# Kernel optimization log

Measured on AMD Instinct MI355X. Metric: run time of the kernel, lower is better.

The kernel has to match this reference:

```python
import jax, jax.numpy as jnp
import numpy as np

N, D, C = 12288, 64, 3
K, GAMMA = 85, 0.5
SAMPLE = 2000


def _safe_sqrt(sq):
    # sqrt with zero gradient at exactly-zero inputs (matches torch cdist/norm backward)
    sq = jnp.maximum(sq, 0.0)
    return jnp.where(sq > 0, jnp.sqrt(jnp.where(sq > 0, sq, 1.0)), 0.0)


def _cdist(a, b):
    # pairwise euclidean distances [Na, Nb]
    sq = jnp.sum(a * a, -1)[:, None] + jnp.sum(b * b, -1)[None, :] - 2.0 * (a @ b.T)
    return _safe_sqrt(sq)


def setup_inputs() -> dict:
    key = jax.random.key(0)
    k1, k2 = jax.random.split(key)
    return {
        "embeddings": jax.random.normal(k1, (N, D), dtype=jnp.float32),
        "coords": jax.random.normal(k2, (N, C), dtype=jnp.float32),
    }


def reference(embeddings, coords):
    n = embeddings.shape[0]
    sample_size = min(n, SAMPLE)
    # deterministic stand-in for torch.randperm sampling
    idx = jax.random.permutation(jax.random.key(42), n)[:sample_size]
    emb_s = embeddings[idx]
    coord_s = coords[idx]

    # Pearson correlation between flattened sample distance matrices
    ed = _cdist(emb_s, emb_s).ravel()
    cd = _cdist(coord_s, coord_s).ravel()
    ec = ed - ed.mean()
    cc = cd - cd.mean()
    es = jnp.sqrt((ec * ec).mean() + 1e-8)
    cs = jnp.sqrt((cc * cc).mean() + 1e-8)
    pearson = (ec * cc).mean() / (es * cs + 1e-8)
    pearson_loss = 1.0 - pearson

    k = min(K, n - 1)
    # KNN in coordinate space, no grad (torch.no_grad)
    coords_ng = jax.lax.stop_gradient(coords)
    full = _cdist(coords_ng, coords_ng)               # [N, N]
    _, knn_idx = jax.lax.top_k(-full, k + 1)          # smallest distances
    knn_idx = knn_idx[:, 1:]                          # drop self -> [N, k]

    nb_emb = embeddings[knn_idx]                      # [N, k, D]
    nb_coord = coords[knn_idx]                        # [N, k, C]
    pred_dist = _safe_sqrt(jnp.sum((embeddings[:, None, :] - nb_emb) ** 2, -1))  # [N, k]
    true_dist = _safe_sqrt(jnp.sum((coords[:, None, :] - nb_coord) ** 2, -1))    # [N, k]
    decay_weight = jnp.exp(-GAMMA * true_dist)
    local_loss = jnp.mean((pred_dist - true_dist) ** 2 * decay_weight)

    return pearson_loss + 0.5 * local_loss
```

## Files before the change

### kernel.cpp

```cpp
#include <hip/hip_runtime.h>
#include <math.h>

#define NPTS 12288
#define DIM 64
#define KNN 85
#define KSEL 86
#define SAMPLE 2000
#define SSTRIDE 6
#define GAMMA 0.5f
#define NT 256
#define WPB 4
#define VIT 12
#define NV 48
#define VCAP 256
#define PT 64
#define PPITCH 68
#define PBLK 1024


struct PearsonS {
  float EqT[DIM][PPITCH];
  float Cp[PT][4];
  float Cq[PT][4];
  float np_[PT];
  float nq_[PT];
  double wred[WPB][5];
};
struct KnnS {
  unsigned h[256];
  unsigned bmax[WPB];
  unsigned long long vkey[VCAP];
  unsigned long long thrkey;
  unsigned vcnt;
};
union SharedU { PearsonS p; KnnS k; };

__global__ void prep_kernel(const float* __restrict__ coord,
                            float* __restrict__ cx, float* __restrict__ cy,
                            float* __restrict__ cz) {
  int j = blockIdx.x * 256 + threadIdx.x;
  if (j < NPTS) {
    cx[j] = coord[3 * j];
    cy[j] = coord[3 * j + 1];
    cz[j] = coord[3 * j + 2];
  }
}

__device__ __forceinline__ void pearson_body(
    SharedU& sh, const float* __restrict__ emb, const float* __restrict__ coord,
    double* __restrict__ acc) {
  const int tid = threadIdx.x;
  const int tx = tid & 15, ty = tid >> 4;
  const int lane = tid & 63, wv = tid >> 6;
  const int pb = blockIdx.x;
  const int p0 = (pb >> 5) * PT, q0 = (pb & 31) * PT;

  for (int e = tid; e < PT * DIM; e += 256) {
    int r = e >> 6, k = e & 63;
    int gq = (q0 + r < SAMPLE ? q0 + r : 0) * SSTRIDE;
    sh.p.EqT[k][r] = emb[(size_t)gq * DIM + k];
  }
  if (tid < PT) {
    int g = (p0 + tid < SAMPLE ? p0 + tid : 0) * SSTRIDE;
    sh.p.Cp[tid][0] = coord[3 * g]; sh.p.Cp[tid][1] = coord[3 * g + 1]; sh.p.Cp[tid][2] = coord[3 * g + 2];
    const float4* E4 = (const float4*)(emb + (size_t)g * DIM);
    float a = 0.f;
    #pragma unroll
    for (int k4 = 0; k4 < DIM / 4; ++k4) {
      float4 v = E4[k4];
      a += v.x * v.x; a += v.y * v.y; a += v.z * v.z; a += v.w * v.w;
    }
    sh.p.np_[tid] = a;
  } else if (tid < 2 * PT) {
    int r = tid - PT;
    int g = (q0 + r < SAMPLE ? q0 + r : 0) * SSTRIDE;
    sh.p.Cq[r][0] = coord[3 * g]; sh.p.Cq[r][1] = coord[3 * g + 1]; sh.p.Cq[r][2] = coord[3 * g + 2];
    const float4* E4 = (const float4*)(emb + (size_t)g * DIM);
    float a = 0.f;
    #pragma unroll
    for (int k4 = 0; k4 < DIM / 4; ++k4) {
      float4 v = E4[k4];
      a += v.x * v.x; a += v.y * v.y; a += v.z * v.z; a += v.w * v.w;
    }
    sh.p.nq_[r] = a;
  }
  __syncthreads();

  const float* rp0; const float* rp1; const float* rp2; const float* rp3;
  {
    int r0 = p0 + 4 * ty;
    int g0 = (r0     < SAMPLE ? r0     : 0) * SSTRIDE;
    int g1 = (r0 + 1 < SAMPLE ? r0 + 1 : 0) * SSTRIDE;
    int g2 = (r0 + 2 < SAMPLE ? r0 + 2 : 0) * SSTRIDE;
    int g3 = (r0 + 3 < SAMPLE ? r0 + 3 : 0) * SSTRIDE;
    rp0 = emb + (size_t)g0 * DIM; rp1 = emb + (size_t)g1 * DIM;
    rp2 = emb + (size_t)g2 * DIM; rp3 = emb + (size_t)g3 * DIM;
  }

  float s[4][4] = {};
  #pragma unroll 16
  for (int k = 0; k < DIM; ++k) {
    float4 eq = *(const float4*)&sh.p.EqT[k][4 * tx];
    float pa[4] = { rp0[k], rp1[k], rp2[k], rp3[k] };
    float qa[4] = { eq.x, eq.y, eq.z, eq.w };
    #pragma unroll
    for (int a = 0; a < 4; ++a)
      #pragma unroll
      for (int b = 0; b < 4; ++b)
        s[a][b] += pa[a] * qa[b];
  }

  const float npr[4] = { sh.p.np_[4 * ty], sh.p.np_[4 * ty + 1], sh.p.np_[4 * ty + 2], sh.p.np_[4 * ty + 3] };
  const float nqr[4] = { sh.p.nq_[4 * tx], sh.p.nq_[4 * tx + 1], sh.p.nq_[4 * tx + 2], sh.p.nq_[4 * tx + 3] };

  double se = 0, sc = 0, se2 = 0, sc2 = 0, sec = 0;
  #pragma unroll
  for (int a = 0; a < 4; ++a)
    #pragma unroll
    for (int b = 0; b < 4; ++b) {
      int p = p0 + 4 * ty + a, q = q0 + 4 * tx + b;
      if (p < SAMPLE && q < SAMPLE) {
        float sq = fmaxf(npr[a] + nqr[b] - 2.f * s[a][b], 0.f);
        float ed = sqrtf(sq);
        float dx = sh.p.Cp[4 * ty + a][0] - sh.p.Cq[4 * tx + b][0];
        float dy = sh.p.Cp[4 * ty + a][1] - sh.p.Cq[4 * tx + b][1];
        float dz = sh.p.Cp[4 * ty + a][2] - sh.p.Cq[4 * tx + b][2];
        float cd = sqrtf(fmaxf(dx * dx + dy * dy + dz * dz, 0.f));
        se += (double)ed; sc += (double)cd;
        se2 += (double)ed * ed; sc2 += (double)cd * cd;
        sec += (double)ed * cd;
      }
    }

  double vals[5] = { se, sc, se2, sc2, sec };
  #pragma unroll
  for (int v = 0; v < 5; ++v) {
    #pragma unroll
    for (int off = 32; off > 0; off >>= 1) vals[v] += __shfl_xor(vals[v], off, 64);
  }
  if (lane == 0) {
    #pragma unroll
    for (int v = 0; v < 5; ++v) sh.p.wred[wv][v] = vals[v];
  }
  __syncthreads();
  if (tid < 5) {
    double sm = sh.p.wred[0][tid] + sh.p.wred[1][tid] + sh.p.wred[2][tid] + sh.p.wred[3][tid];
    atomicAdd(&acc[tid], sm);
  }
}

__device__ __forceinline__ void knn_body(
    SharedU& sh, const float* __restrict__ emb, const float* __restrict__ cx,
    const float* __restrict__ cy, const float* __restrict__ cz,
    double* __restrict__ acc) {
  const int i = blockIdx.x - PBLK;
  const int tid = threadIdx.x;
  const int lane = tid & 63;
  const int wv = tid >> 6;

  const float qx = cx[i], qy = cy[i], qz = cz[i];
  const float4* CX4 = (const float4*)cx;
  const float4* CY4 = (const float4*)cy;
  const float4* CZ4 = (const float4*)cz;

  unsigned dp[NV / 2];
  unsigned m1 = 0xFFFFu, m2 = 0xFFFFu;
  #pragma unroll
  for (int it = 0; it < VIT; ++it) {
    int idx = it * NT + tid;
    float4 x4 = CX4[idx], y4 = CY4[idx], z4 = CZ4[idx];
    float dx, dy, dz;
    dx = qx - x4.x; dy = qy - y4.x; dz = qz - z4.x;
    unsigned t0 = __float_as_uint(dx * dx + dy * dy + dz * dz) >> 16;
    dx = qx - x4.y; dy = qy - y4.y; dz = qz - z4.y;
    unsigned t1 = __float_as_uint(dx * dx + dy * dy + dz * dz) >> 16;
    dx = qx - x4.z; dy = qy - y4.z; dz = qz - z4.z;
    unsigned t2 = __float_as_uint(dx * dx + dy * dy + dz * dz) >> 16;
    dx = qx - x4.w; dy = qy - y4.w; dz = qz - z4.w;
    unsigned t3 = __float_as_uint(dx * dx + dy * dy + dz * dz) >> 16;
    dp[2 * it]     = t0 | (t1 << 16);
    dp[2 * it + 1] = t2 | (t3 << 16);
    unsigned hi;
    hi = t0 > m1 ? t0 : m1; m1 = t0 < m1 ? t0 : m1; m2 = hi < m2 ? hi : m2;
    hi = t1 > m1 ? t1 : m1; m1 = t1 < m1 ? t1 : m1; m2 = hi < m2 ? hi : m2;
    hi = t2 > m1 ? t2 : m1; m1 = t2 < m1 ? t2 : m1; m2 = hi < m2 ? hi : m2;
    hi = t3 > m1 ? t3 : m1; m1 = t3 < m1 ? t3 : m1; m2 = hi < m2 ? hi : m2;
  }
  const float4 ei4 = ((const float4*)(emb + (size_t)i * DIM))[lane & 15];

  unsigned M2w = m2;
  #pragma unroll
  for (int off = 32; off > 0; off >>= 1) {
    unsigned t2_ = __shfl_xor((int)M2w, off, 64);
    M2w = t2_ > M2w ? t2_ : M2w;
  }
  if (lane == 0) sh.k.bmax[wv] = M2w;
  sh.k.h[tid] = 0;
  if (tid == 0) { sh.k.vcnt = 0; sh.k.thrkey = 0xFFFFFFFFFFFFFFFFULL; }
  __syncthreads();

  const unsigned b0 = sh.k.bmax[0], b1 = sh.k.bmax[1];
  const unsigned b2_ = sh.k.bmax[2], b3 = sh.k.bmax[3];
  unsigned Bu = b0 < b1 ? b0 : b1;
  unsigned Bu2 = b2_ < b3 ? b2_ : b3;
  Bu = Bu < Bu2 ? Bu : Bu2;
  const float sbin = 256.0f / (float)(Bu + 1);

  #pragma unroll
  for (int t2i = 0; t2i < NV / 2; ++t2i) {
    unsigned pk = dp[t2i];
    unsigned ua = pk & 0xFFFFu, ub = pk >> 16;
    if (ua <= Bu) {
      int bb = (int)((float)ua * sbin);
      atomicAdd(&sh.k.h[bb > 255 ? 255 : bb], 1u);
    }
    if (ub <= Bu) {
      int bb = (int)((float)ub * sbin);
      atomicAdd(&sh.k.h[bb > 255 ? 255 : bb], 1u);
    }
  }
  __syncthreads();

  unsigned c0 = sh.k.h[4 * lane], c1 = sh.k.h[4 * lane + 1];
  unsigned c2 = sh.k.h[4 * lane + 2], c3 = sh.k.h[4 * lane + 3];
  unsigned lt = c0 + c1 + c2 + c3;
  unsigned incl = lt;
  #pragma unroll
  for (int off = 1; off < 64; off <<= 1) {
    unsigned t2_ = __shfl_up(incl, off, 64);
    if (lane >= off) incl += t2_;
  }
  unsigned excl = incl - lt;
  bool has = (lt > 0) && (excl < KSEL) && (KSEL <= incl);
  unsigned bin = 4 * lane, cum = excl;
  if (cum + c0 >= KSEL) { bin = 4 * lane; }
  else { cum += c0;
    if (cum + c1 >= KSEL) { bin = 4 * lane + 1; }
    else { cum += c1;
      if (cum + c2 >= KSEL) { bin = 4 * lane + 2; }
      else { bin = 4 * lane + 3; } } }
  unsigned long long bal = __ballot(has);
  int src = __ffsll((unsigned long long)bal) - 1;
  const unsigned bsel = (unsigned)__shfl((int)bin, src, 64);

  #pragma unroll
  for (int t = 0; t < NV; ++t) {
    unsigned pk = dp[t >> 1];
    unsigned ut = (t & 1) ? (pk >> 16) : (pk & 0xFFFFu);
    int bb = (int)((float)ut * sbin);
    if (bb <= (int)bsel) {
      int j = 4 * ((t >> 2) * NT + tid) + (t & 3);
      float dx = qx - cx[j], dy = qy - cy[j], dz = qz - cz[j];
      unsigned u = __float_as_uint(dx * dx + dy * dy + dz * dz);
      unsigned pos = atomicAdd(&sh.k.vcnt, 1u);
      if (pos < VCAP)
        sh.k.vkey[pos] = ((unsigned long long)u << 14) | (unsigned)j;
    }
  }
  __syncthreads();
  const unsigned vc = sh.k.vcnt;
  const int tot = (int)(vc < VCAP ? vc : VCAP);

  if (tid < tot) {
    const unsigned long long kt = sh.k.vkey[tid];
    int rank = 0;
    for (int k = 0; k < tot; ++k) rank += (sh.k.vkey[k] < kt) ? 1 : 0;
    if (rank == KSEL - 1) sh.k.thrkey = kt;
  }
  __syncthreads();
  const unsigned long long thr64 = sh.k.thrkey;

  const int q = lane >> 4;
  const int l16 = lane & 15;
  float lsum = 0.f;
  for (int base = wv * 4; base < tot; base += 16) {
    int idx = base + q;
    bool valid = false;
    unsigned u = 0; int j = 0;
    if (idx < tot) {
      unsigned long long kk64 = sh.k.vkey[idx];
      u = (unsigned)(kk64 >> 14);
      j = (int)(kk64 & 0x3FFFu);
      valid = (kk64 <= thr64) && (j != i);
    }
    float s = 0.f;
    if (valid) {
      float4 e4 = ((const float4*)(emb + (size_t)j * DIM))[l16];
      float d0 = ei4.x - e4.x, d1 = ei4.y - e4.y;
      float d2 = ei4.z - e4.z, d3 = ei4.w - e4.w;
      s = d0 * d0 + d1 * d1 + d2 * d2 + d3 * d3;
    }
    s += __shfl_xor(s, 1, 64);
    s += __shfl_xor(s, 2, 64);
    s += __shfl_xor(s, 4, 64);
    s += __shfl_xor(s, 8, 64);
    if (valid && l16 == 0) {
      float td = sqrtf(__uint_as_float(u));
      float pd = sqrtf(fmaxf(s, 0.f));
      float diff = pd - td;
      lsum += diff * diff * expf(-GAMMA * td);
    }
  }
  #pragma unroll
  for (int off = 32; off > 0; off >>= 1) lsum += __shfl_xor(lsum, off, 64);
  if (lane == 0) atomicAdd(&acc[5 + (i & 7) * 4 + wv], (double)lsum);
}

__global__ __launch_bounds__(NT) void fused_kernel(
    const float* __restrict__ emb, const float* __restrict__ coord,
    const float* __restrict__ cx, const float* __restrict__ cy,
    const float* __restrict__ cz, double* __restrict__ acc) {
  __shared__ SharedU sh;
  if (blockIdx.x < PBLK) {
    pearson_body(sh, emb, coord, acc);
  } else {
    knn_body(sh, emb, cx, cy, cz, acc);
  }
}

__global__ void finalize_kernel(const double* __restrict__ acc,
                                float* __restrict__ out) {
  double M = (double)SAMPLE * (double)SAMPLE;
  double med = acc[0] / M, mcd = acc[1] / M;
  double ve = acc[2] / M - med * med;
  double vc = acc[3] / M - mcd * mcd;
  double es = sqrt(ve + 1e-8);
  double cs = sqrt(vc + 1e-8);
  double cov = acc[4] / M - med * mcd;
  double pearson = cov / (es * cs + 1e-8);
  double lsum = 0.0;
  for (int s = 5; s < 37; ++s) lsum += acc[s];
  double local = lsum / ((double)NPTS * (double)KNN);
  out[0] = (float)((1.0 - pearson) + 0.5 * local);
}

extern "C" void kernel_launch(void* const* d_in, const int* in_sizes, int n_in,
                              void* d_out, int out_size, void* d_ws, size_t ws_size,
                              hipStream_t stream) {
  const float* emb = (const float*)d_in[0];
  const float* coord = (const float*)d_in[1];
  double* acc = (double*)d_ws;
  float* cx = (float*)((char*)d_ws + 512);
  float* cy = cx + NPTS;
  float* cz = cy + NPTS;

  hipMemsetAsync(d_ws, 0, 37 * sizeof(double), stream);

  prep_kernel<<<(NPTS + 255) / 256, 256, 0, stream>>>(coord, cx, cy, cz);

  fused_kernel<<<PBLK + NPTS, NT, 0, stream>>>(emb, coord, cx, cy, cz, acc);

  finalize_kernel<<<1, 1, 0, stream>>>(acc, (float*)d_out);
}
```

Before: 330.1 us.

## Screen KNN candidates with packed fp16 distances and per-thread minimum histogram

```diff
diff --git a/kernel.cpp b/kernel.cpp
--- a/kernel.cpp
+++ b/kernel.cpp
@@ -10,12 +10,14 @@
 #define GAMMA 0.5f
 #define NT 256
 #define WPB 4
-#define VIT 12
-#define NV 48
-#define VCAP 256
+#define HIT 6
+#define NP 24
+#define VCAP 320
 #define PT 64
 #define PPITCH 68
 #define PBLK 1024
+
+typedef _Float16 hf2 __attribute__((ext_vector_type(2)));
 
 
 struct PearsonS {
@@ -37,12 +39,13 @@
 
 __global__ void prep_kernel(const float* __restrict__ coord,
                             float* __restrict__ cx, float* __restrict__ cy,
-                            float* __restrict__ cz) {
+                            float* __restrict__ cz, _Float16* __restrict__ hx,
+                            _Float16* __restrict__ hy, _Float16* __restrict__ hz) {
   int j = blockIdx.x * 256 + threadIdx.x;
   if (j < NPTS) {
-    cx[j] = coord[3 * j];
-    cy[j] = coord[3 * j + 1];
-    cz[j] = coord[3 * j + 2];
+    float x = coord[3 * j], y = coord[3 * j + 1], z = coord[3 * j + 2];
+    cx[j] = x; cy[j] = y; cz[j] = z;
+    hx[j] = (_Float16)x; hy[j] = (_Float16)y; hz[j] = (_Float16)z;
   }
 }
 
@@ -152,72 +155,75 @@
 __device__ __forceinline__ void knn_body(
     SharedU& sh, const float* __restrict__ emb, const float* __restrict__ cx,
     const float* __restrict__ cy, const float* __restrict__ cz,
-    double* __restrict__ acc) {
+    const _Float16* __restrict__ hx, const _Float16* __restrict__ hy,
+    const _Float16* __restrict__ hz, double* __restrict__ acc) {
   const int i = blockIdx.x - PBLK;
   const int tid = threadIdx.x;
   const int lane = tid & 63;
   const int wv = tid >> 6;
 
   const float qx = cx[i], qy = cy[i], qz = cz[i];
-  const float4* CX4 = (const float4*)cx;
-  const float4* CY4 = (const float4*)cy;
-  const float4* CZ4 = (const float4*)cz;
-
-  unsigned dp[NV / 2];
-  unsigned m1 = 0xFFFFu, m2 = 0xFFFFu;
-  #pragma unroll
-  for (int it = 0; it < VIT; ++it) {
+  const hf2 qx2 = { (_Float16)qx, (_Float16)qx };
+  const hf2 qy2 = { (_Float16)qy, (_Float16)qy };
+  const hf2 qz2 = { (_Float16)qz, (_Float16)qz };
+  const uint4* HX = (const uint4*)hx;
+  const uint4* HY = (const uint4*)hy;
+  const uint4* HZ = (const uint4*)hz;
+
+  unsigned dp[NP];
+  hf2 m1p = { (_Float16)65504.f, (_Float16)65504.f };
+#define DSTEP(UX, UY, UZ, T)                                   \
+  {                                                            \
+    hf2 x2 = __builtin_bit_cast(hf2, UX);                      \
+    hf2 y2 = __builtin_bit_cast(hf2, UY);                      \
+    hf2 z2 = __builtin_bit_cast(hf2, UZ);                      \
+    hf2 dx = qx2 - x2, dy = qy2 - y2, dz = qz2 - z2;           \
+    hf2 s = dx * dx; s += dy * dy; s += dz * dz;               \
+    dp[T] = __builtin_bit_cast(unsigned, s);                   \
+    m1p = __builtin_elementwise_min(m1p, s);                   \
+  }
+  #pragma unroll
+  for (int it = 0; it < HIT; ++it) {
     int idx = it * NT + tid;
-    float4 x4 = CX4[idx], y4 = CY4[idx], z4 = CZ4[idx];
-    float dx, dy, dz;
-    dx = qx - x4.x; dy = qy - y4.x; dz = qz - z4.x;
-    unsigned t0 = __float_as_uint(dx * dx + dy * dy + dz * dz) >> 16;
-    dx = qx - x4.y; dy = qy - y4.y; dz = qz - z4.y;
-    unsigned t1 = __float_as_uint(dx * dx + dy * dy + dz * dz) >> 16;
-    dx = qx - x4.z; dy = qy - y4.z; dz = qz - z4.z;
-    unsigned t2 = __float_as_uint(dx * dx + dy * dy + dz * dz) >> 16;
-    dx = qx - x4.w; dy = qy - y4.w; dz = qz - z4.w;
-    unsigned t3 = __float_as_uint(dx * dx + dy * dy + dz * dz) >> 16;
-    dp[2 * it]     = t0 | (t1 << 16);
-    dp[2 * it + 1] = t2 | (t3 << 16);
-    unsigned hi;
-    hi = t0 > m1 ? t0 : m1; m1 = t0 < m1 ? t0 : m1; m2 = hi < m2 ? hi : m2;
-    hi = t1 > m1 ? t1 : m1; m1 = t1 < m1 ? t1 : m1; m2 = hi < m2 ? hi : m2;
-    hi = t2 > m1 ? t2 : m1; m1 = t2 < m1 ? t2 : m1; m2 = hi < m2 ? hi : m2;
-    hi = t3 > m1 ? t3 : m1; m1 = t3 < m1 ? t3 : m1; m2 = hi < m2 ? hi : m2;
-  }
+    uint4 wx = HX[idx], wy = HY[idx], wz = HZ[idx];
+    DSTEP(wx.x, wy.x, wz.x, 4 * it + 0)
+    DSTEP(wx.y, wy.y, wz.y, 4 * it + 1)
+    DSTEP(wx.z, wy.z, wz.z, 4 * it + 2)
+    DSTEP(wx.w, wy.w, wz.w, 4 * it + 3)
+  }
+#undef DSTEP
   const float4 ei4 = ((const float4*)(emb + (size_t)i * DIM))[lane & 15];
 
-  unsigned M2w = m2;
+  unsigned m1u;
+  {
+    _Float16 a0 = m1p.x, a1 = m1p.y;
+    _Float16 mh = a0 < a1 ? a0 : a1;
+    m1u = (unsigned)__builtin_bit_cast(unsigned short, mh);
+  }
+  unsigned Mw = m1u;
   #pragma unroll
   for (int off = 32; off > 0; off >>= 1) {
-    unsigned t2_ = __shfl_xor((int)M2w, off, 64);
-    M2w = t2_ > M2w ? t2_ : M2w;
-  }
-  if (lane == 0) sh.k.bmax[wv] = M2w;
+    unsigned t2 = __shfl_xor((int)Mw, off, 64);
+    Mw = t2 > Mw ? t2 : Mw;
+  }
+  if (lane == 0) sh.k.bmax[wv] = Mw;
   sh.k.h[tid] = 0;
   if (tid == 0) { sh.k.vcnt = 0; sh.k.thrkey = 0xFFFFFFFFFFFFFFFFULL; }
   __syncthreads();
 
-  const unsigned b0 = sh.k.bmax[0], b1 = sh.k.bmax[1];
-  const unsigned b2_ = sh.k.bmax[2], b3 = sh.k.bmax[3];
-  unsigned Bu = b0 < b1 ? b0 : b1;
-  unsigned Bu2 = b2_ < b3 ? b2_ : b3;
-  Bu = Bu < Bu2 ? Bu : Bu2;
+  unsigned Bu;
+  {
+    unsigned b0 = sh.k.bmax[0], b1 = sh.k.bmax[1];
+    unsigned b2_ = sh.k.bmax[2], b3 = sh.k.bmax[3];
+    unsigned a = b0 < b1 ? b0 : b1, b = b0 < b1 ? b1 : b0;
+    unsigned c = b2_ < b3 ? b2_ : b3, d = b2_ < b3 ? b3 : b2_;
+    Bu = (a < c) ? (b < c ? b : c) : (d < a ? d : a);
+  }
   const float sbin = 256.0f / (float)(Bu + 1);
 
-  #pragma unroll
-  for (int t2i = 0; t2i < NV / 2; ++t2i) {
-    unsigned pk = dp[t2i];
-    unsigned ua = pk & 0xFFFFu, ub = pk >> 16;
-    if (ua <= Bu) {
-      int bb = (int)((float)ua * sbin);
-      atomicAdd(&sh.k.h[bb > 255 ? 255 : bb], 1u);
-    }
-    if (ub <= Bu) {
-      int bb = (int)((float)ub * sbin);
-      atomicAdd(&sh.k.h[bb > 255 ? 255 : bb], 1u);
-    }
+  if (m1u <= Bu) {
+    int bb = (int)((float)m1u * sbin);
+    atomicAdd(&sh.k.h[bb > 255 ? 255 : bb], 1u);
   }
   __syncthreads();
 
@@ -227,8 +233,8 @@
   unsigned incl = lt;
   #pragma unroll
   for (int off = 1; off < 64; off <<= 1) {
-    unsigned t2_ = __shfl_up(incl, off, 64);
-    if (lane >= off) incl += t2_;
+    unsigned t2 = __shfl_up(incl, off, 64);
+    if (lane >= off) incl += t2;
   }
   unsigned excl = incl - lt;
   bool has = (lt > 0) && (excl < KSEL) && (KSEL <= incl);
@@ -243,18 +249,28 @@
   int src = __ffsll((unsigned long long)bal) - 1;
   const unsigned bsel = (unsigned)__shfl((int)bin, src, 64);
 
-  #pragma unroll
-  for (int t = 0; t < NV; ++t) {
-    unsigned pk = dp[t >> 1];
-    unsigned ut = (t & 1) ? (pk >> 16) : (pk & 0xFFFFu);
-    int bb = (int)((float)ut * sbin);
-    if (bb <= (int)bsel) {
-      int j = 4 * ((t >> 2) * NT + tid) + (t & 3);
-      float dx = qx - cx[j], dy = qy - cy[j], dz = qz - cz[j];
+  unsigned U16 = (((bsel + 1) * (Bu + 1) + 255) >> 8) + 128;
+  if (U16 > 65535u) U16 = 65535u;
+
+  #pragma unroll
+  for (int t = 0; t < NP; ++t) {
+    unsigned pk = dp[t];
+    unsigned lo = pk & 0xFFFFu, hi = pk >> 16;
+    int j0 = 8 * ((t >> 2) * NT + tid) + 2 * (t & 3);
+    if (lo <= U16) {
+      float dx = qx - cx[j0], dy = qy - cy[j0], dz = qz - cz[j0];
       unsigned u = __float_as_uint(dx * dx + dy * dy + dz * dz);
       unsigned pos = atomicAdd(&sh.k.vcnt, 1u);
       if (pos < VCAP)
-        sh.k.vkey[pos] = ((unsigned long long)u << 14) | (unsigned)j;
+        sh.k.vkey[pos] = ((unsigned long long)u << 14) | (unsigned)j0;
+    }
+    if (hi <= U16) {
+      int j1 = j0 + 1;
+      float dx = qx - cx[j1], dy = qy - cy[j1], dz = qz - cz[j1];
+      unsigned u = __float_as_uint(dx * dx + dy * dy + dz * dz);
+      unsigned pos = atomicAdd(&sh.k.vcnt, 1u);
+      if (pos < VCAP)
+        sh.k.vkey[pos] = ((unsigned long long)u << 14) | (unsigned)j1;
     }
   }
   __syncthreads();
@@ -309,12 +325,14 @@
 __global__ __launch_bounds__(NT) void fused_kernel(
     const float* __restrict__ emb, const float* __restrict__ coord,
     const float* __restrict__ cx, const float* __restrict__ cy,
-    const float* __restrict__ cz, double* __restrict__ acc) {
+    const float* __restrict__ cz, const _Float16* __restrict__ hx,
+    const _Float16* __restrict__ hy, const _Float16* __restrict__ hz,
+    double* __restrict__ acc) {
   __shared__ SharedU sh;
   if (blockIdx.x < PBLK) {
     pearson_body(sh, emb, coord, acc);
   } else {
-    knn_body(sh, emb, cx, cy, cz, acc);
+    knn_body(sh, emb, cx, cy, cz, hx, hy, hz, acc);
   }
 }
 
@@ -343,12 +361,15 @@
   float* cx = (float*)((char*)d_ws + 512);
   float* cy = cx + NPTS;
   float* cz = cy + NPTS;
+  _Float16* hx = (_Float16*)(cz + NPTS);
+  _Float16* hy = hx + NPTS;
+  _Float16* hz = hy + NPTS;
 
   hipMemsetAsync(d_ws, 0, 37 * sizeof(double), stream);
 
-  prep_kernel<<<(NPTS + 255) / 256, 256, 0, stream>>>(coord, cx, cy, cz);
-
-  fused_kernel<<<PBLK + NPTS, NT, 0, stream>>>(emb, coord, cx, cy, cz, acc);
+  prep_kernel<<<(NPTS + 255) / 256, 256, 0, stream>>>(coord, cx, cy, cz, hx, hy, hz);
+
+  fused_kernel<<<PBLK + NPTS, NT, 0, stream>>>(emb, coord, cx, cy, cz, hx, hy, hz, acc);
 
   finalize_kernel<<<1, 1, 0, stream>>>(acc, (float*)d_out);
 }
```

After: 338.6 us. +2.6%, slower.

## Drop SoA prep and finalize kernels; fuse finalize via last-block counter

Applied to the files above, without the earlier changes.

```diff
diff --git a/kernel.cpp b/kernel.cpp
--- a/kernel.cpp
+++ b/kernel.cpp
@@ -16,6 +16,7 @@
 #define PT 64
 #define PPITCH 68
 #define PBLK 1024
+#define GRID (PBLK + NPTS)
 
 
 struct PearsonS {
@@ -35,17 +36,6 @@
 };
 union SharedU { PearsonS p; KnnS k; };
 
-__global__ void prep_kernel(const float* __restrict__ coord,
-                            float* __restrict__ cx, float* __restrict__ cy,
-                            float* __restrict__ cz) {
-  int j = blockIdx.x * 256 + threadIdx.x;
-  if (j < NPTS) {
-    cx[j] = coord[3 * j];
-    cy[j] = coord[3 * j + 1];
-    cz[j] = coord[3 * j + 2];
-  }
-}
-
 __device__ __forceinline__ void pearson_body(
     SharedU& sh, const float* __restrict__ emb, const float* __restrict__ coord,
     double* __restrict__ acc) {
@@ -150,33 +140,30 @@
 }
 
 __device__ __forceinline__ void knn_body(
-    SharedU& sh, const float* __restrict__ emb, const float* __restrict__ cx,
-    const float* __restrict__ cy, const float* __restrict__ cz,
+    SharedU& sh, const float* __restrict__ emb, const float* __restrict__ coord,
     double* __restrict__ acc) {
   const int i = blockIdx.x - PBLK;
   const int tid = threadIdx.x;
   const int lane = tid & 63;
   const int wv = tid >> 6;
 
-  const float qx = cx[i], qy = cy[i], qz = cz[i];
-  const float4* CX4 = (const float4*)cx;
-  const float4* CY4 = (const float4*)cy;
-  const float4* CZ4 = (const float4*)cz;
+  const float qx = coord[3 * i], qy = coord[3 * i + 1], qz = coord[3 * i + 2];
+  const float4* C4 = (const float4*)coord;
 
   unsigned dp[NV / 2];
   unsigned m1 = 0xFFFFu, m2 = 0xFFFFu;
   #pragma unroll
   for (int it = 0; it < VIT; ++it) {
     int idx = it * NT + tid;
-    float4 x4 = CX4[idx], y4 = CY4[idx], z4 = CZ4[idx];
+    float4 a = C4[3 * idx], b = C4[3 * idx + 1], c = C4[3 * idx + 2];
     float dx, dy, dz;
-    dx = qx - x4.x; dy = qy - y4.x; dz = qz - z4.x;
+    dx = qx - a.x; dy = qy - a.y; dz = qz - a.z;
     unsigned t0 = __float_as_uint(dx * dx + dy * dy + dz * dz) >> 16;
-    dx = qx - x4.y; dy = qy - y4.y; dz = qz - z4.y;
+    dx = qx - a.w; dy = qy - b.x; dz = qz - b.y;
     unsigned t1 = __float_as_uint(dx * dx + dy * dy + dz * dz) >> 16;
-    dx = qx - x4.z; dy = qy - y4.z; dz = qz - z4.z;
+    dx = qx - b.z; dy = qy - b.w; dz = qz - c.x;
     unsigned t2 = __float_as_uint(dx * dx + dy * dy + dz * dz) >> 16;
-    dx = qx - x4.w; dy = qy - y4.w; dz = qz - z4.w;
+    dx = qx - c.y; dy = qy - c.z; dz = qz - c.w;
     unsigned t3 = __float_as_uint(dx * dx + dy * dy + dz * dz) >> 16;
     dp[2 * it]     = t0 | (t1 << 16);
     dp[2 * it + 1] = t2 | (t3 << 16);
@@ -250,7 +237,8 @@
     int bb = (int)((float)ut * sbin);
     if (bb <= (int)bsel) {
       int j = 4 * ((t >> 2) * NT + tid) + (t & 3);
-      float dx = qx - cx[j], dy = qy - cy[j], dz = qz - cz[j];
+      float dx = qx - coord[3 * j], dy = qy - coord[3 * j + 1];
+      float dz = qz - coord[3 * j + 2];
       unsigned u = __float_as_uint(dx * dx + dy * dy + dz * dz);
       unsigned pos = atomicAdd(&sh.k.vcnt, 1u);
       if (pos < VCAP)
@@ -308,30 +296,38 @@
 
 __global__ __launch_bounds__(NT) void fused_kernel(
     const float* __restrict__ emb, const float* __restrict__ coord,
-    const float* __restrict__ cx, const float* __restrict__ cy,
-    const float* __restrict__ cz, double* __restrict__ acc) {
+    double* __restrict__ acc, unsigned* __restrict__ done,
+    float* __restrict__ out) {
   __shared__ SharedU sh;
   if (blockIdx.x < PBLK) {
     pearson_body(sh, emb, coord, acc);
   } else {
-    knn_body(sh, emb, cx, cy, cz, acc);
-  }
-}
-
-__global__ void finalize_kernel(const double* __restrict__ acc,
-                                float* __restrict__ out) {
-  double M = (double)SAMPLE * (double)SAMPLE;
-  double med = acc[0] / M, mcd = acc[1] / M;
-  double ve = acc[2] / M - med * med;
-  double vc = acc[3] / M - mcd * mcd;
-  double es = sqrt(ve + 1e-8);
-  double cs = sqrt(vc + 1e-8);
-  double cov = acc[4] / M - med * mcd;
-  double pearson = cov / (es * cs + 1e-8);
-  double lsum = 0.0;
-  for (int s = 5; s < 37; ++s) lsum += acc[s];
-  double local = lsum / ((double)NPTS * (double)KNN);
-  out[0] = (float)((1.0 - pearson) + 0.5 * local);
+    knn_body(sh, emb, coord, acc);
+  }
+
+  __threadfence();
+  if (threadIdx.x == 0) {
+    unsigned prev = __atomic_fetch_add(done, 1u, __ATOMIC_RELAXED);
+    if (prev == (unsigned)(GRID - 1)) {
+      __threadfence();
+      double a[37];
+      #pragma unroll 1
+      for (int s = 0; s < 37; ++s) a[s] = atomicAdd(&acc[s], 0.0);
+      double M = (double)SAMPLE * (double)SAMPLE;
+      double med = a[0] / M, mcd = a[1] / M;
+      double ve = a[2] / M - med * med;
+      double vc = a[3] / M - mcd * mcd;
+      double es = sqrt(ve + 1e-8);
+      double cs = sqrt(vc + 1e-8);
+      double cov = a[4] / M - med * mcd;
+      double pearson = cov / (es * cs + 1e-8);
+      double lsum = 0.0;
+      #pragma unroll 1
+      for (int s = 5; s < 37; ++s) lsum += a[s];
+      double local = lsum / ((double)NPTS * (double)KNN);
+      out[0] = (float)((1.0 - pearson) + 0.5 * local);
+    }
+  }
 }
 
 extern "C" void kernel_launch(void* const* d_in, const int* in_sizes, int n_in,
@@ -340,15 +336,9 @@
   const float* emb = (const float*)d_in[0];
   const float* coord = (const float*)d_in[1];
   double* acc = (double*)d_ws;
-  float* cx = (float*)((char*)d_ws + 512);
-  float* cy = cx + NPTS;
-  float* cz = cy + NPTS;
-
-  hipMemsetAsync(d_ws, 0, 37 * sizeof(double), stream);
-
-  prep_kernel<<<(NPTS + 255) / 256, 256, 0, stream>>>(coord, cx, cy, cz);
-
-  fused_kernel<<<PBLK + NPTS, NT, 0, stream>>>(emb, coord, cx, cy, cz, acc);
-
-  finalize_kernel<<<1, 1, 0, stream>>>(acc, (float*)d_out);
+  unsigned* done = (unsigned*)((char*)d_ws + 296);
+
+  hipMemsetAsync(d_ws, 0, 512, stream);
+
+  fused_kernel<<<GRID, NT, 0, stream>>>(emb, coord, acc, done, (float*)d_out);
 }
```

After: 1.060 ms. +221.2%, slower.
